# Kernel optimization log

Hardware: AMD Instinct MI355X
Metric: run time of the kernel (lower is better)

The kernel has to match this reference:

```python
import jax, jax.numpy as jnp
import numpy as np

EMBED_DIM = 1024
HEAD_DIM = 64


def setup_inputs() -> dict:
    key = jax.random.key(0)
    ks = jax.random.split(key, 9)
    B, S, E, H = 4, 2048, EMBED_DIM, HEAD_DIM
    s = 1.0 / np.sqrt(E)
    return {
        "query": jax.random.normal(ks[0], (B, S, E), dtype=jnp.float32),
        "key": jax.random.normal(ks[1], (B, S, E), dtype=jnp.float32),
        "value": jax.random.normal(ks[2], (B, S, E), dtype=jnp.float32),
        "Wq": jax.random.normal(ks[3], (E, H), dtype=jnp.float32) * s,
        "bq": jnp.zeros((H,), dtype=jnp.float32),
        "Wk": jax.random.normal(ks[4], (E, H), dtype=jnp.float32) * s,
        "bk": jnp.zeros((H,), dtype=jnp.float32),
        "Wv": jax.random.normal(ks[5], (E, H), dtype=jnp.float32) * s,
        "bv": jnp.zeros((H,), dtype=jnp.float32),
    }


def reference(query, key, value, Wq, bq, Wk, bk, Wv, bv):
    # per-head linear projections: [B,S,E] @ [E,H] -> [B,S,H]
    q = jnp.einsum("bse,eh->bsh", query, Wq) + bq
    k = jnp.einsum("bse,eh->bsh", key, Wk) + bk
    v = jnp.einsum("bse,eh->bsh", value, Wv) + bv
    # NOTE: original code computes dim_k but never scales -> unscaled scores
    scores = jnp.einsum("bqh,bkh->bqk", q, k)  # [B,S,S]
    weights = jax.nn.softmax(scores, axis=-1)
    return jnp.einsum("bqk,bkh->bqh", weights, v)  # [B,S,H]
```

## Files before the change

### kernel.cpp

```cpp
#include <hip/hip_runtime.h>
#include <math.h>

#define B 4
#define S 2048
#define E 1024
#define H 64
#define BS (B*S)
#define LOG2E 1.44269504088896f
#define CINIT (-69.2493662f)

typedef float v4f __attribute__((ext_vector_type(4)));
typedef short v8s __attribute__((ext_vector_type(8)));
typedef unsigned short u16;
typedef u16 u16x8 __attribute__((ext_vector_type(8)));

#define MFMA(a,b,c) __builtin_amdgcn_mfma_f32_16x16x32_bf16(a,b,c,0,0,0)

__device__ inline u16 rh_bf16(float x){ return (u16)((__float_as_uint(x)+0x8000u)>>16); }

__global__ __launch_bounds__(256) void wsetup_kernel(
    const float* __restrict__ Wq, const float* __restrict__ Wk,
    const float* __restrict__ Wv,
    u16* __restrict__ Wt_hi, u16* __restrict__ Wt_lo)
{
    __shared__ float wt[64][65];
    const int t  = threadIdx.x;
    const int p  = blockIdx.x >> 4;
    const int e0 = (blockIdx.x & 15) * 64;
    const float* Wsrc = (p==0) ? Wq : (p==1 ? Wk : Wv);
    const float scale = (p==0) ? LOG2E : 1.0f;

    #pragma unroll
    for (int i=0;i<16;i++){
        int e_l = i*4 + (t>>6);
        wt[e_l][t&63] = Wsrc[(size_t)(e0+e_l)*H + (t&63)] * scale;
    }
    __syncthreads();

    const int h = t>>2, e16 = (t&3)*16;
    u16 hi_a[16], lo_a[16];
    #pragma unroll
    for (int j=0;j<16;j++){
        float f = wt[e16+j][h];
        unsigned u = __float_as_uint(f);
        hi_a[j] = (u16)(u>>16);
        float hif = __uint_as_float(u & 0xFFFF0000u);
        lo_a[j] = rh_bf16(f - hif);
    }
    u16* dh = Wt_hi + (size_t)(p*64+h)*E + e0 + e16;
    u16* dl = Wt_lo + (size_t)(p*64+h)*E + e0 + e16;
    *(u16x8*)dh     = *(u16x8*)&hi_a[0];
    *(u16x8*)(dh+8) = *(u16x8*)&hi_a[8];
    *(u16x8*)dl     = *(u16x8*)&lo_a[0];
    *(u16x8*)(dl+8) = *(u16x8*)&lo_a[8];
}

__global__ __launch_bounds__(128) void proj_kernel(
    const float* __restrict__ query, const float* __restrict__ key_,
    const float* __restrict__ value,
    const u16* __restrict__ Wt_hi, const u16* __restrict__ Wt_lo,
    const float* __restrict__ bq, const float* __restrict__ bk,
    const float* __restrict__ bv,
    u16* __restrict__ q_hi, u16* __restrict__ q_lo,
    u16* __restrict__ k_hi, u16* __restrict__ k_lo,
    u16* __restrict__ v_bf)
{
    __shared__ __align__(16) u16 xh[32][72], xl[32][72];
    __shared__ __align__(16) u16 wh[64][72], wl[64][72];

    const int t  = threadIdx.x;
    const int p  = blockIdx.x >> 8;
    const int r0 = (blockIdx.x & 255) * 32;
    const float* xp = (p==0) ? query : (p==1 ? key_ : value);
    const int wv = t>>6, lane = t&63, m = lane&15, quad = lane>>4;

    const int srow = t>>2, se16 = (t&3)*16;
    const int swh  = t>>1, seo  = (t&1)*32;

    v4f acc[4];
    #pragma unroll
    for (int nt=0;nt<4;nt++) acc[nt] = (v4f){0.f,0.f,0.f,0.f};

    for (int ec=0; ec<16; ec++){
        const int e0 = ec*64;
        __syncthreads();
        {
            const float* xr = xp + (size_t)(r0+srow)*E + e0 + se16;
            float4 aa[4];
            aa[0] = *(const float4*)(xr);
            aa[1] = *(const float4*)(xr+4);
            aa[2] = *(const float4*)(xr+8);
            aa[3] = *(const float4*)(xr+12);
            float fv[16];
            #pragma unroll
            for (int q4=0;q4<4;q4++){
                fv[q4*4+0]=aa[q4].x; fv[q4*4+1]=aa[q4].y;
                fv[q4*4+2]=aa[q4].z; fv[q4*4+3]=aa[q4].w;
            }
            u16 ha[16], la[16];
            #pragma unroll
            for (int j=0;j<16;j++){
                unsigned u = __float_as_uint(fv[j]);
                ha[j] = (u16)(u>>16);
                la[j] = rh_bf16(fv[j] - __uint_as_float(u & 0xFFFF0000u));
            }
            *(u16x8*)&xh[srow][se16]   = *(u16x8*)&ha[0];
            *(u16x8*)&xh[srow][se16+8] = *(u16x8*)&ha[8];
            *(u16x8*)&xl[srow][se16]   = *(u16x8*)&la[0];
            *(u16x8*)&xl[srow][se16+8] = *(u16x8*)&la[8];
        }
        {
            const u16* sh = Wt_hi + (size_t)(p*64+swh)*E + e0 + seo;
            const u16* sl = Wt_lo + (size_t)(p*64+swh)*E + e0 + seo;
            #pragma unroll
            for (int i=0;i<4;i++){
                *(u16x8*)&wh[swh][seo + i*8] = *(const u16x8*)(sh + i*8);
                *(u16x8*)&wl[swh][seo + i*8] = *(const u16x8*)(sl + i*8);
            }
        }
        __syncthreads();

        v8s ah0 = *(v8s*)&xh[wv*16+m][quad*8];
        v8s ah1 = *(v8s*)&xh[wv*16+m][32+quad*8];
        v8s al0 = *(v8s*)&xl[wv*16+m][quad*8];
        v8s al1 = *(v8s*)&xl[wv*16+m][32+quad*8];
        #pragma unroll
        for (int nt=0;nt<4;nt++){
            v8s bh0 = *(v8s*)&wh[nt*16+m][quad*8];
            v8s bh1 = *(v8s*)&wh[nt*16+m][32+quad*8];
            v8s bl0 = *(v8s*)&wl[nt*16+m][quad*8];
            v8s bl1 = *(v8s*)&wl[nt*16+m][32+quad*8];
            v4f d = acc[nt];
            d = MFMA(ah0,bh0,d); d = MFMA(ah1,bh1,d);
            d = MFMA(al0,bh0,d); d = MFMA(al1,bh1,d);
            d = MFMA(ah0,bl0,d); d = MFMA(ah1,bl1,d);
            acc[nt] = d;
        }
    }

    const float* bp = (p==0) ? bq : (p==1 ? bk : bv);
    const float bscale = (p==0) ? LOG2E : 1.0f;
    #pragma unroll
    for (int nt=0;nt<4;nt++){
        const int hl = nt*16+m;
        const float bb = bp[hl]*bscale;
        #pragma unroll
        for (int r=0;r<4;r++){
            const int gr = r0 + wv*16 + quad*4 + r;
            const float val = acc[nt][r] + bb;
            if (p<2){
                unsigned u = __float_as_uint(val);
                u16 hi = (u16)(u>>16);
                float hif = __uint_as_float(u & 0xFFFF0000u);
                u16 lo = rh_bf16(val - hif);
                u16* dh = (p==0) ? q_hi : k_hi;
                u16* dl = (p==0) ? q_lo : k_lo;
                dh[(size_t)gr*H + hl] = hi;
                dl[(size_t)gr*H + hl] = lo;
            } else {
                v_bf[(size_t)gr*H + hl] = rh_bf16(val);
            }
        }
    }
}

__global__ __launch_bounds__(256) void vtrans_kernel(
    const u16* __restrict__ v_bf, u16* __restrict__ vt)
{
    __shared__ __align__(16) u16 tl[64][72];
    const int t = threadIdx.x;
    const int b = blockIdx.x >> 5, s0 = (blockIdx.x & 31)*64;
    {
        const int r = t>>2, c16 = (t&3)*16;
        const u16* src = v_bf + (size_t)(b*S + s0 + r)*H + c16;
        *(u16x8*)&tl[r][c16]   = *(const u16x8*)src;
        *(u16x8*)&tl[r][c16+8] = *(const u16x8*)(src+8);
    }
    __syncthreads();
    const int h = t>>2, s16 = (t&3)*16;
    u16 oa[16];
    #pragma unroll
    for (int j=0;j<16;j++) oa[j] = tl[s16+j][h];
    u16* dst = vt + (size_t)(b*H + h)*S + s0 + s16;
    *(u16x8*)dst     = *(u16x8*)&oa[0];
    *(u16x8*)(dst+8) = *(u16x8*)&oa[8];
}

__global__ __launch_bounds__(256) void attn_kernel(
    const u16* __restrict__ qh_g, const u16* __restrict__ ql_g,
    const u16* __restrict__ kh_g, const u16* __restrict__ kl_g,
    const u16* __restrict__ vt_g,
    float* __restrict__ accw, float* __restrict__ lw, int ksplit)
{
    __shared__ __align__(16) u16 khe[2][16][72];
    __shared__ __align__(16) u16 kle[2][16][72];
    __shared__ __align__(16) u16 vtl[64][40];
    __shared__ __align__(16) u16 pl[4][16][40];

    const int t = threadIdx.x;
    const int wv = t>>6, lane = t&63, m = lane&15, quad = lane>>4;
    const int bid = blockIdx.x;
    const int qb = bid / ksplit, chunk = bid % ksplit;
    const int b = qb >> 5, s0 = (qb & 31)*64;
    const int ck = S / ksplit;
    const int j0base = chunk * ck;
    const int iters = ck / 32;

    const u16* qr = qh_g + (size_t)(b*S + s0 + wv*16 + m)*H + quad*8;
    const u16* qrl = ql_g + (size_t)(b*S + s0 + wv*16 + m)*H + quad*8;
    const v8s qh0 = *(const v8s*)(qr),  qh1 = *(const v8s*)(qr+32);
    const v8s ql0 = *(const v8s*)(qrl), ql1 = *(const v8s*)(qrl+32);

    v4f oacc[4];
    #pragma unroll
    for (int nt=0;nt<4;nt++) oacc[nt] = (v4f){0.f,0.f,0.f,0.f};
    float lp[4] = {0.f,0.f,0.f,0.f};
    const v4f cinit = (v4f){CINIT,CINIT,CINIT,CINIT};

    const int sj = t>>3, sh8 = (t&7)*8;
    const u16* khs = kh_g + (size_t)(b*S + j0base + sj)*H + sh8;
    const u16* kls = kl_g + (size_t)(b*S + j0base + sj)*H + sh8;
    u16* khd = &khe[sj&1][sj>>1][sh8];
    u16* kld = &kle[sj&1][sj>>1][sh8];
    const int vh = t>>2, vj8 = (t&3)*8;
    const u16* vts = vt_g + (size_t)(b*H + vh)*S + j0base + vj8;
    u16* vtd = &vtl[vh][vj8];

    for (int it=0; it<iters; ++it){
        __syncthreads();
        *(u16x8*)khd = *(const u16x8*)(khs + (size_t)it*32*H);
        *(u16x8*)kld = *(const u16x8*)(kls + (size_t)it*32*H);
        *(u16x8*)vtd = *(const u16x8*)(vts + it*32);
        __syncthreads();

        v4f sc[2];
        #pragma unroll
        for (int jt=0;jt<2;jt++){
            const u16* kr  = &khe[jt][m][quad*8];
            const u16* krl = &kle[jt][m][quad*8];
            v8s b0 = *(const v8s*)kr,  b1 = *(const v8s*)(kr+32);
            v8s c0 = *(const v8s*)krl, c1 = *(const v8s*)(krl+32);
            v4f d = cinit;
            d = MFMA(qh0,b0,d); d = MFMA(qh1,b1,d);
            d = MFMA(ql0,b0,d); d = MFMA(ql1,b1,d);
            d = MFMA(qh0,c0,d); d = MFMA(qh1,c1,d);
            sc[jt] = d;
        }

        #pragma unroll
        for (int r=0;r<4;r++){
            float p0 = exp2f(sc[0][r]);
            float p1 = exp2f(sc[1][r]);
            lp[r] += p0 + p1;
            unsigned pk = ((__float_as_uint(p0)+0x8000u)>>16)
                        | ((__float_as_uint(p1)+0x8000u) & 0xFFFF0000u);
            *(unsigned*)&pl[wv][quad*4+r][2*m] = pk;
        }
        __syncthreads();

        v8s pa = *(const v8s*)&pl[wv][m][quad*8];
        #pragma unroll
        for (int nt=0;nt<4;nt++){
            v8s vb = *(const v8s*)&vtl[nt*16+m][quad*8];
            oacc[nt] = MFMA(pa, vb, oacc[nt]);
        }
    }

    #pragma unroll
    for (int r=0;r<4;r++){
        float v = lp[r];
        v += __shfl_xor(v,1); v += __shfl_xor(v,2);
        v += __shfl_xor(v,4); v += __shfl_xor(v,8);
        lp[r] = v;
    }
    const int growb = b*S + s0 + wv*16;
    if (m==0){
        float4 lv; lv.x=lp[0]; lv.y=lp[1]; lv.z=lp[2]; lv.w=lp[3];
        *(float4*)(lw + (size_t)chunk*BS + growb + quad*4) = lv;
    }
    float* ab = accw + ((size_t)chunk*BS + growb)*H;
    #pragma unroll
    for (int nt=0;nt<4;nt++){
        #pragma unroll
        for (int r=0;r<4;r++)
            ab[(size_t)(quad*4+r)*H + nt*16 + m] = oacc[nt][r];
    }
}

__global__ __launch_bounds__(256) void merge_kernel(
    const float* __restrict__ accw, const float* __restrict__ lw,
    float* __restrict__ out, int ksplit)
{
    const int idx = blockIdx.x*256 + threadIdx.x;
    const int row = idx >> 4, h4 = (idx & 15)*4;
    float4 a = {0.f,0.f,0.f,0.f};
    float ls = 0.f;
    for (int c=0;c<ksplit;c++){
        const float4 t4 = *(const float4*)(accw + ((size_t)c*BS + row)*H + h4);
        a.x+=t4.x; a.y+=t4.y; a.z+=t4.z; a.w+=t4.w;
        ls += lw[(size_t)c*BS + row];
    }
    const float inv = __builtin_amdgcn_rcpf(ls);
    float4 o; o.x=a.x*inv; o.y=a.y*inv; o.z=a.z*inv; o.w=a.w*inv;
    *(float4*)(out + (size_t)row*H + h4) = o;
}

extern "C" void kernel_launch(void* const* d_in, const int* in_sizes, int n_in,
                              void* d_out, int out_size, void* d_ws, size_t ws_size,
                              hipStream_t stream) {
    const float* query = (const float*)d_in[0];
    const float* key_  = (const float*)d_in[1];
    const float* value = (const float*)d_in[2];
    const float* Wq    = (const float*)d_in[3];
    const float* bq    = (const float*)d_in[4];
    const float* Wk    = (const float*)d_in[5];
    const float* bk    = (const float*)d_in[6];
    const float* Wv    = (const float*)d_in[7];
    const float* bv    = (const float*)d_in[8];
    float* out = (float*)d_out;

    char* base = (char*)d_ws;
    size_t off = 0;
    u16* Wt_hi = (u16*)(base + off); off += (size_t)3*64*E*2;
    u16* Wt_lo = (u16*)(base + off); off += (size_t)3*64*E*2;
    u16* q_hi  = (u16*)(base + off); off += (size_t)BS*H*2;
    u16* q_lo  = (u16*)(base + off); off += (size_t)BS*H*2;
    u16* k_hi  = (u16*)(base + off); off += (size_t)BS*H*2;
    u16* k_lo  = (u16*)(base + off); off += (size_t)BS*H*2;
    u16* v_bf  = (u16*)(base + off); off += (size_t)BS*H*2;
    u16* vt    = (u16*)(base + off); off += (size_t)BS*H*2;
    const size_t fixed = off;
    const size_t CH = (size_t)BS*H*4 + (size_t)BS*4;

    int K = 1;
    if      (ws_size >= fixed + 8*CH) K = 8;
    else if (ws_size >= fixed + 4*CH) K = 4;
    else if (ws_size >= fixed + 2*CH) K = 2;

    float* lw   = (float*)(base + fixed);
    float* accw = (float*)(base + fixed + (size_t)K*BS*4);

    wsetup_kernel<<<48, 256, 0, stream>>>(Wq, Wk, Wv, Wt_hi, Wt_lo);
    proj_kernel<<<768, 128, 0, stream>>>(query, key_, value, Wt_hi, Wt_lo,
                                         bq, bk, bv, q_hi, q_lo, k_hi, k_lo, v_bf);
    vtrans_kernel<<<128, 256, 0, stream>>>(v_bf, vt);
    attn_kernel<<<128*K, 256, 0, stream>>>(q_hi, q_lo, k_hi, k_lo, vt, accw, lw, K);
    merge_kernel<<<512, 256, 0, stream>>>(accw, lw, out, K);
}
```

Baseline: 173.2 us.

## Prefetch tiles in projection and attention, fuse V transpose, widen key tiles

The projection kernel now runs 256 threads, walks the E dimension in 128-wide chunks, and prefetches the next chunk's x and W values into registers while the current chunk is multiplied. It also writes V already transposed through a shared-memory tile, so the separate vtrans kernel and the v_bf buffer are removed. The attention kernel processes 64 keys per iteration, prefetches the next K/V tile into registers, and drops one __syncthreads per iteration around the P buffer. This is meant to cut load latency, barrier count and one kernel launch, in exchange for higher register and LDS use.

```diff
diff --git a/kernel.cpp b/kernel.cpp
--- a/kernel.cpp
+++ b/kernel.cpp
@@ -12,7 +12,10 @@
 typedef float v4f __attribute__((ext_vector_type(4)));
 typedef short v8s __attribute__((ext_vector_type(8)));
 typedef unsigned short u16;
+typedef unsigned int u32;
+typedef unsigned long long u64;
 typedef u16 u16x8 __attribute__((ext_vector_type(8)));
+typedef u16 u16x4 __attribute__((ext_vector_type(4)));
 
 #define MFMA(a,b,c) __builtin_amdgcn_mfma_f32_16x16x32_bf16(a,b,c,0,0,0)
 
@@ -55,7 +58,7 @@
     *(u16x8*)(dl+8) = *(u16x8*)&lo_a[8];
 }
 
-__global__ __launch_bounds__(128) void proj_kernel(
+__global__ __launch_bounds__(256, 3) void proj_kernel(
     const float* __restrict__ query, const float* __restrict__ key_,
     const float* __restrict__ value,
     const u16* __restrict__ Wt_hi, const u16* __restrict__ Wt_lo,
@@ -63,40 +66,52 @@
     const float* __restrict__ bv,
     u16* __restrict__ q_hi, u16* __restrict__ q_lo,
     u16* __restrict__ k_hi, u16* __restrict__ k_lo,
-    u16* __restrict__ v_bf)
+    u16* __restrict__ vt)
 {
-    __shared__ __align__(16) u16 xh[32][72], xl[32][72];
-    __shared__ __align__(16) u16 wh[64][72], wl[64][72];
+    __shared__ __align__(16) u16 smem[26112];
+    u16 (*xh)[136] = (u16(*)[136])&smem[0];
+    u16 (*xl)[136] = (u16(*)[136])&smem[4352];
+    u16 (*wh)[136] = (u16(*)[136])&smem[8704];
+    u16 (*wl)[136] = (u16(*)[136])&smem[17408];
+    u16 (*vtile)[40] = (u16(*)[40])&smem[0];
 
     const int t  = threadIdx.x;
     const int p  = blockIdx.x >> 8;
     const int r0 = (blockIdx.x & 255) * 32;
     const float* xp = (p==0) ? query : (p==1 ? key_ : value);
     const int wv = t>>6, lane = t&63, m = lane&15, quad = lane>>4;
-
-    const int srow = t>>2, se16 = (t&3)*16;
-    const int swh  = t>>1, seo  = (t&1)*32;
-
-    v4f acc[4];
-    #pragma unroll
-    for (int nt=0;nt<4;nt++) acc[nt] = (v4f){0.f,0.f,0.f,0.f};
-
-    for (int ec=0; ec<16; ec++){
-        const int e0 = ec*64;
+    const int whalf = wv>>1, nh = wv&1;
+
+    const int sxr = t>>3, sxc = (t&7)*16;
+    const int swr = t>>2, swc = (t&3)*32;
+    const float* xb  = xp + (size_t)(r0+sxr)*E + sxc;
+    const u16*   shb = Wt_hi + (size_t)(p*64+swr)*E + swc;
+    const u16*   slb = Wt_lo + (size_t)(p*64+swr)*E + swc;
+
+    v4f acc[2];
+    acc[0] = (v4f){0.f,0.f,0.f,0.f};
+    acc[1] = (v4f){0.f,0.f,0.f,0.f};
+
+    float4 xr_[4];
+    u16x8  whr_[4], wlr_[4];
+
+#define LOADP(PH) {                                                            \
+        _Pragma("unroll")                                                      \
+        for (int j=0;j<4;j++) xr_[j]  = *(const float4*)(xb  + (PH)*128 + j*4);\
+        _Pragma("unroll")                                                      \
+        for (int j=0;j<4;j++) whr_[j] = *(const u16x8*)(shb + (PH)*128 + j*8); \
+        _Pragma("unroll")                                                      \
+        for (int j=0;j<4;j++) wlr_[j] = *(const u16x8*)(slb + (PH)*128 + j*8); \
+    }
+
+    LOADP(0);
+    for (int ph=0; ph<8; ++ph){
         __syncthreads();
         {
-            const float* xr = xp + (size_t)(r0+srow)*E + e0 + se16;
-            float4 aa[4];
-            aa[0] = *(const float4*)(xr);
-            aa[1] = *(const float4*)(xr+4);
-            aa[2] = *(const float4*)(xr+8);
-            aa[3] = *(const float4*)(xr+12);
-            float fv[16];
-            #pragma unroll
-            for (int q4=0;q4<4;q4++){
-                fv[q4*4+0]=aa[q4].x; fv[q4*4+1]=aa[q4].y;
-                fv[q4*4+2]=aa[q4].z; fv[q4*4+3]=aa[q4].w;
-            }
+            float fv[16] = {xr_[0].x,xr_[0].y,xr_[0].z,xr_[0].w,
+                            xr_[1].x,xr_[1].y,xr_[1].z,xr_[1].w,
+                            xr_[2].x,xr_[2].y,xr_[2].z,xr_[2].w,
+                            xr_[3].x,xr_[3].y,xr_[3].z,xr_[3].w};
             u16 ha[16], la[16];
             #pragma unroll
             for (int j=0;j<16;j++){
@@ -104,98 +119,88 @@
                 ha[j] = (u16)(u>>16);
                 la[j] = rh_bf16(fv[j] - __uint_as_float(u & 0xFFFF0000u));
             }
-            *(u16x8*)&xh[srow][se16]   = *(u16x8*)&ha[0];
-            *(u16x8*)&xh[srow][se16+8] = *(u16x8*)&ha[8];
-            *(u16x8*)&xl[srow][se16]   = *(u16x8*)&la[0];
-            *(u16x8*)&xl[srow][se16+8] = *(u16x8*)&la[8];
-        }
-        {
-            const u16* sh = Wt_hi + (size_t)(p*64+swh)*E + e0 + seo;
-            const u16* sl = Wt_lo + (size_t)(p*64+swh)*E + e0 + seo;
+            *(u16x8*)&xh[sxr][sxc]   = *(u16x8*)&ha[0];
+            *(u16x8*)&xh[sxr][sxc+8] = *(u16x8*)&ha[8];
+            *(u16x8*)&xl[sxr][sxc]   = *(u16x8*)&la[0];
+            *(u16x8*)&xl[sxr][sxc+8] = *(u16x8*)&la[8];
+        }
+        #pragma unroll
+        for (int j=0;j<4;j++) *(u16x8*)&wh[swr][swc + j*8] = whr_[j];
+        #pragma unroll
+        for (int j=0;j<4;j++) *(u16x8*)&wl[swr][swc + j*8] = wlr_[j];
+        __syncthreads();
+        if (ph+1 < 8) LOADP(ph+1);
+        const int arow = whalf*16 + m;
+        #pragma unroll
+        for (int s=0; s<4; ++s){
+            v8s ah = *(const v8s*)&xh[arow][s*32+quad*8];
+            v8s al = *(const v8s*)&xl[arow][s*32+quad*8];
             #pragma unroll
-            for (int i=0;i<4;i++){
-                *(u16x8*)&wh[swh][seo + i*8] = *(const u16x8*)(sh + i*8);
-                *(u16x8*)&wl[swh][seo + i*8] = *(const u16x8*)(sl + i*8);
+            for (int i=0;i<2;i++){
+                const int wrow = (nh*2+i)*16 + m;
+                v8s bh = *(const v8s*)&wh[wrow][s*32+quad*8];
+                v8s bl = *(const v8s*)&wl[wrow][s*32+quad*8];
+                v4f d = acc[i];
+                d = MFMA(ah,bh,d);
+                d = MFMA(al,bh,d);
+                d = MFMA(ah,bl,d);
+                acc[i] = d;
             }
         }
-        __syncthreads();
-
-        v8s ah0 = *(v8s*)&xh[wv*16+m][quad*8];
-        v8s ah1 = *(v8s*)&xh[wv*16+m][32+quad*8];
-        v8s al0 = *(v8s*)&xl[wv*16+m][quad*8];
-        v8s al1 = *(v8s*)&xl[wv*16+m][32+quad*8];
-        #pragma unroll
-        for (int nt=0;nt<4;nt++){
-            v8s bh0 = *(v8s*)&wh[nt*16+m][quad*8];
-            v8s bh1 = *(v8s*)&wh[nt*16+m][32+quad*8];
-            v8s bl0 = *(v8s*)&wl[nt*16+m][quad*8];
-            v8s bl1 = *(v8s*)&wl[nt*16+m][32+quad*8];
-            v4f d = acc[nt];
-            d = MFMA(ah0,bh0,d); d = MFMA(ah1,bh1,d);
-            d = MFMA(al0,bh0,d); d = MFMA(al1,bh1,d);
-            d = MFMA(ah0,bl0,d); d = MFMA(ah1,bl1,d);
-            acc[nt] = d;
-        }
-    }
+    }
+#undef LOADP
 
     const float* bp = (p==0) ? bq : (p==1 ? bk : bv);
-    const float bscale = (p==0) ? LOG2E : 1.0f;
-    #pragma unroll
-    for (int nt=0;nt<4;nt++){
-        const int hl = nt*16+m;
-        const float bb = bp[hl]*bscale;
-        #pragma unroll
-        for (int r=0;r<4;r++){
-            const int gr = r0 + wv*16 + quad*4 + r;
-            const float val = acc[nt][r] + bb;
-            if (p<2){
+    if (p<2){
+        const float bscale = (p==0) ? LOG2E : 1.0f;
+        u16* dh = (p==0) ? q_hi : k_hi;
+        u16* dl = (p==0) ? q_lo : k_lo;
+        #pragma unroll
+        for (int i=0;i<2;i++){
+            const int hl = nh*32 + i*16 + m;
+            const float bb = bp[hl]*bscale;
+            #pragma unroll
+            for (int r=0;r<4;r++){
+                const int gr = r0 + whalf*16 + quad*4 + r;
+                const float val = acc[i][r] + bb;
                 unsigned u = __float_as_uint(val);
                 u16 hi = (u16)(u>>16);
                 float hif = __uint_as_float(u & 0xFFFF0000u);
                 u16 lo = rh_bf16(val - hif);
-                u16* dh = (p==0) ? q_hi : k_hi;
-                u16* dl = (p==0) ? q_lo : k_lo;
                 dh[(size_t)gr*H + hl] = hi;
                 dl[(size_t)gr*H + hl] = lo;
-            } else {
-                v_bf[(size_t)gr*H + hl] = rh_bf16(val);
             }
         }
-    }
-}
-
-__global__ __launch_bounds__(256) void vtrans_kernel(
-    const u16* __restrict__ v_bf, u16* __restrict__ vt)
-{
-    __shared__ __align__(16) u16 tl[64][72];
-    const int t = threadIdx.x;
-    const int b = blockIdx.x >> 5, s0 = (blockIdx.x & 31)*64;
-    {
-        const int r = t>>2, c16 = (t&3)*16;
-        const u16* src = v_bf + (size_t)(b*S + s0 + r)*H + c16;
-        *(u16x8*)&tl[r][c16]   = *(const u16x8*)src;
-        *(u16x8*)&tl[r][c16+8] = *(const u16x8*)(src+8);
-    }
-    __syncthreads();
-    const int h = t>>2, s16 = (t&3)*16;
-    u16 oa[16];
-    #pragma unroll
-    for (int j=0;j<16;j++) oa[j] = tl[s16+j][h];
-    u16* dst = vt + (size_t)(b*H + h)*S + s0 + s16;
-    *(u16x8*)dst     = *(u16x8*)&oa[0];
-    *(u16x8*)(dst+8) = *(u16x8*)&oa[8];
-}
-
-__global__ __launch_bounds__(256) void attn_kernel(
+    } else {
+        __syncthreads();
+        const int rlb = whalf*16 + quad*4;
+        #pragma unroll
+        for (int i=0;i<2;i++){
+            const int hl = nh*32 + i*16 + m;
+            const float bb = bp[hl];
+            u16 vv[4];
+            #pragma unroll
+            for (int r=0;r<4;r++) vv[r] = rh_bf16(acc[i][r] + bb);
+            *(u16x4*)&vtile[hl][rlb] = *(u16x4*)&vv[0];
+        }
+        __syncthreads();
+        const int h = t>>2, so = (t&3)*8;
+        const int bidx = r0 >> 11, s0l = r0 & (S-1);
+        u16* dst = vt + ((size_t)(bidx*H + h))*S + s0l + so;
+        *(u16x8*)dst = *(const u16x8*)&vtile[h][so];
+    }
+}
+
+__global__ __launch_bounds__(256, 4) void attn_kernel(
     const u16* __restrict__ qh_g, const u16* __restrict__ ql_g,
     const u16* __restrict__ kh_g, const u16* __restrict__ kl_g,
     const u16* __restrict__ vt_g,
     float* __restrict__ accw, float* __restrict__ lw, int ksplit)
 {
-    __shared__ __align__(16) u16 khe[2][16][72];
-    __shared__ __align__(16) u16 kle[2][16][72];
-    __shared__ __align__(16) u16 vtl[64][40];
-    __shared__ __align__(16) u16 pl[4][16][40];
+    __shared__ __align__(16) u16 khe[4][16][72];
+    __shared__ __align__(16) u16 kle[4][16][72];
+    __shared__ __align__(16) u16 vtl[64][72];
+    __shared__ __align__(16) u16 pl[4][16][72];
 
     const int t = threadIdx.x;
     const int wv = t>>6, lane = t&63, m = lane&15, quad = lane>>4;
@@ -204,7 +209,7 @@
     const int b = qb >> 5, s0 = (qb & 31)*64;
     const int ck = S / ksplit;
     const int j0base = chunk * ck;
-    const int iters = ck / 32;
+    const int iters = ck >> 6;
 
     const u16* qr = qh_g + (size_t)(b*S + s0 + wv*16 + m)*H + quad*8;
     const u16* qrl = ql_g + (size_t)(b*S + s0 + wv*16 + m)*H + quad*8;
@@ -217,25 +222,37 @@
     float lp[4] = {0.f,0.f,0.f,0.f};
     const v4f cinit = (v4f){CINIT,CINIT,CINIT,CINIT};
 
-    const int sj = t>>3, sh8 = (t&7)*8;
-    const u16* khs = kh_g + (size_t)(b*S + j0base + sj)*H + sh8;
-    const u16* kls = kl_g + (size_t)(b*S + j0base + sj)*H + sh8;
-    u16* khd = &khe[sj&1][sj>>1][sh8];
-    u16* kld = &kle[sj&1][sj>>1][sh8];
-    const int vh = t>>2, vj8 = (t&3)*8;
-    const u16* vts = vt_g + (size_t)(b*H + vh)*S + j0base + vj8;
-    u16* vtd = &vtl[vh][vj8];
+    const int sj = t>>2, sh = (t&3)*16;
+    const u16* khs = kh_g + (size_t)(b*S + j0base + sj)*H + sh;
+    const u16* kls = kl_g + (size_t)(b*S + j0base + sj)*H + sh;
+    u16* khd = &khe[sj&3][sj>>2][sh];
+    u16* kld = &kle[sj&3][sj>>2][sh];
+    const int vh = t>>2, vj = (t&3)*16;
+    const u16* vts = vt_g + (size_t)(b*H + vh)*S + j0base + vj;
+    u16* vtd = &vtl[vh][vj];
+
+    u16x8 khp[2], klp[2], vtp[2];
+    khp[0] = *(const u16x8*)khs;  khp[1] = *(const u16x8*)(khs+8);
+    klp[0] = *(const u16x8*)kls;  klp[1] = *(const u16x8*)(kls+8);
+    vtp[0] = *(const u16x8*)vts;  vtp[1] = *(const u16x8*)(vts+8);
 
     for (int it=0; it<iters; ++it){
         __syncthreads();
-        *(u16x8*)khd = *(const u16x8*)(khs + (size_t)it*32*H);
-        *(u16x8*)kld = *(const u16x8*)(kls + (size_t)it*32*H);
-        *(u16x8*)vtd = *(const u16x8*)(vts + it*32);
-        __syncthreads();
-
-        v4f sc[2];
-        #pragma unroll
-        for (int jt=0;jt<2;jt++){
+        *(u16x8*)khd = khp[0];  *(u16x8*)(khd+8) = khp[1];
+        *(u16x8*)kld = klp[0];  *(u16x8*)(kld+8) = klp[1];
+        *(u16x8*)vtd = vtp[0];  *(u16x8*)(vtd+8) = vtp[1];
+        __syncthreads();
+        if (it+1 < iters){
+            const u16* kh2 = khs + (size_t)(it+1)*64*H;
+            const u16* kl2 = kls + (size_t)(it+1)*64*H;
+            const u16* vt2 = vts + (it+1)*64;
+            khp[0] = *(const u16x8*)kh2;  khp[1] = *(const u16x8*)(kh2+8);
+            klp[0] = *(const u16x8*)kl2;  klp[1] = *(const u16x8*)(kl2+8);
+            vtp[0] = *(const u16x8*)vt2;  vtp[1] = *(const u16x8*)(vt2+8);
+        }
+        v4f sc[4];
+        #pragma unroll
+        for (int jt=0;jt<4;jt++){
             const u16* kr  = &khe[jt][m][quad*8];
             const u16* krl = &kle[jt][m][quad*8];
             v8s b0 = *(const v8s*)kr,  b1 = *(const v8s*)(kr+32);
@@ -246,23 +263,29 @@
             d = MFMA(qh0,c0,d); d = MFMA(qh1,c1,d);
             sc[jt] = d;
         }
-
         #pragma unroll
         for (int r=0;r<4;r++){
             float p0 = exp2f(sc[0][r]);
             float p1 = exp2f(sc[1][r]);
-            lp[r] += p0 + p1;
-            unsigned pk = ((__float_as_uint(p0)+0x8000u)>>16)
-                        | ((__float_as_uint(p1)+0x8000u) & 0xFFFF0000u);
-            *(unsigned*)&pl[wv][quad*4+r][2*m] = pk;
-        }
-        __syncthreads();
-
-        v8s pa = *(const v8s*)&pl[wv][m][quad*8];
+            float p2 = exp2f(sc[2][r]);
+            float p3 = exp2f(sc[3][r]);
+            lp[r] += (p0 + p1) + (p2 + p3);
+            u32 pkA = ((__float_as_uint(p0)+0x8000u)>>16)
+                    | ((__float_as_uint(p1)+0x8000u) & 0xFFFF0000u);
+            u32 pkB = ((__float_as_uint(p2)+0x8000u)>>16)
+                    | ((__float_as_uint(p3)+0x8000u) & 0xFFFF0000u);
+            *(u64*)&pl[wv][quad*4+r][4*m] = (u64)pkA | ((u64)pkB << 32);
+        }
+        v8s pa0 = *(const v8s*)&pl[wv][m][quad*8];
+        v8s pa1 = *(const v8s*)&pl[wv][m][32+quad*8];
         #pragma unroll
         for (int nt=0;nt<4;nt++){
-            v8s vb = *(const v8s*)&vtl[nt*16+m][quad*8];
-            oacc[nt] = MFMA(pa, vb, oacc[nt]);
+            v8s vb0 = *(const v8s*)&vtl[nt*16+m][quad*8];
+            v8s vb1 = *(const v8s*)&vtl[nt*16+m][32+quad*8];
+            v4f d = oacc[nt];
+            d = MFMA(pa0, vb0, d);
+            d = MFMA(pa1, vb1, d);
+            oacc[nt] = d;
         }
     }
 
@@ -327,7 +350,6 @@
     u16* q_lo  = (u16*)(base + off); off += (size_t)BS*H*2;
     u16* k_hi  = (u16*)(base + off); off += (size_t)BS*H*2;
     u16* k_lo  = (u16*)(base + off); off += (size_t)BS*H*2;
-    u16* v_bf  = (u16*)(base + off); off += (size_t)BS*H*2;
     u16* vt    = (u16*)(base + off); off += (size_t)BS*H*2;
     const size_t fixed = off;
     const size_t CH = (size_t)BS*H*4 + (size_t)BS*4;
@@ -341,9 +363,8 @@
     float* accw = (float*)(base + fixed + (size_t)K*BS*4);
 
     wsetup_kernel<<<48, 256, 0, stream>>>(Wq, Wk, Wv, Wt_hi, Wt_lo);
-    proj_kernel<<<768, 128, 0, stream>>>(query, key_, value, Wt_hi, Wt_lo,
-                                         bq, bk, bv, q_hi, q_lo, k_hi, k_lo, v_bf);
-    vtrans_kernel<<<128, 256, 0, stream>>>(v_bf, vt);
+    proj_kernel<<<768, 256, 0, stream>>>(query, key_, value, Wt_hi, Wt_lo,
+                                         bq, bk, bv, q_hi, q_lo, k_hi, k_lo, vt);
     attn_kernel<<<128*K, 256, 0, stream>>>(q_hi, q_lo, k_hi, k_lo, vt, accw, lw, K);
     merge_kernel<<<512, 256, 0, stream>>>(accw, lw, out, K);
 }
```

Result: faster. 169.0 us (-2.4%).
